# Performance work log

Measured on AMD Instinct MI355X. Metric: run time of the kernel, lower is better.

Reference implementation:

```python
import jax, jax.numpy as jnp
import numpy as np

B, S, D, H = 4, 1024, 1024, 16
HS = D // H  # head_size = 64


def setup_inputs() -> dict:
    key = jax.random.key(0)
    ks = jax.random.split(key, 12)
    sc_d = 1.0 / np.sqrt(D)
    sc_h = 1.0 / np.sqrt(HS)
    inp = {
        "queries": jax.random.normal(ks[0], (B, S, D), jnp.float32),
        "keys": jax.random.normal(ks[1], (B, S, D), jnp.float32),
        "values": jax.random.normal(ks[2], (B, S, D), jnp.float32),
        # causal mask: scores where mask == 0 are filled with -1e9
        "mask": jnp.tril(jnp.ones((S, S), jnp.int32)),
        # per-head query/key projections: [H, D, HS] weights, [H, HS] biases
        "Wq": jax.random.uniform(ks[3], (H, D, HS), jnp.float32, -sc_d, sc_d),
        "bq": jax.random.uniform(ks[4], (H, HS), jnp.float32, -sc_d, sc_d),
        "Wk": jax.random.uniform(ks[5], (H, D, HS), jnp.float32, -sc_d, sc_d),
        "bk": jax.random.uniform(ks[6], (H, HS), jnp.float32, -sc_d, sc_d),
        # shared value projection: [D, HS]
        "Wv": jax.random.uniform(ks[7], (D, HS), jnp.float32, -sc_d, sc_d),
        "bv": jax.random.uniform(ks[8], (HS,), jnp.float32, -sc_d, sc_d),
        # output projection: [HS, D]
        "Wo": jax.random.uniform(ks[9], (HS, D), jnp.float32, -sc_h, sc_h),
        "bo": jax.random.uniform(ks[10], (D,), jnp.float32, -sc_h, sc_h),
    }
    return inp


def reference(queries, keys, values, mask, Wq, bq, Wk, bk, Wv, bv, Wo, bo):
    # shared value projection: [B, S, HS]
    v = jnp.einsum("bsd,de->bse", values, Wv) + bv
    # batched per-head projections (replaces the python loop over heads)
    q = jnp.einsum("bsd,hde->bhse", queries, Wq) + bq[None, :, None, :]
    k = jnp.einsum("btd,hde->bhte", keys, Wk) + bk[None, :, None, :]
    scores = jnp.einsum("bhse,bhte->bhst", q, k) / jnp.sqrt(jnp.float32(HS))
    scores = jnp.where(mask == 0, jnp.float32(-1e9), scores)
    attn = jax.nn.softmax(scores, axis=-1)  # [B, H, S, S]; dropout = eval-mode identity
    head_out = jnp.einsum("bhst,bte->bhse", attn, v)
    out = head_out.mean(axis=1)  # mean over heads -> [B, S, HS]
    out = jnp.einsum("bse,ed->bsd", out, Wo) + bo
    attention_weights = attn.mean(axis=1)  # [B, S, S]
    return out, attention_weights
```

## Files before the change

kernel.cpp:

```cpp
#include <hip/hip_runtime.h>
#include <hip/hip_bf16.h>
#include <stdint.h>

typedef _Float16 half8 __attribute__((ext_vector_type(8)));
typedef _Float16 half4 __attribute__((ext_vector_type(4)));
typedef float    f32x4 __attribute__((ext_vector_type(4)));

#define MFMA16(a, b, c) __builtin_amdgcn_mfma_f32_16x16x32_f16(a, b, c, 0, 0, 0)

__global__ __launch_bounds__(256) void transpose_to_f16(
    const float* __restrict__ X, _Float16* __restrict__ Y,
    int R, int C, long inBS, long outBS)
{
    __shared__ float t[32][33];
    const int bz = blockIdx.z;
    X += (long)bz * inBS;
    Y += (long)bz * outBS;
    const int c0 = blockIdx.x * 32, r0 = blockIdx.y * 32;
    const int tx = threadIdx.x & 31, ty = threadIdx.x >> 5;
#pragma unroll
    for (int i = 0; i < 4; ++i)
        t[ty + i * 8][tx] = X[(long)(r0 + ty + i * 8) * C + c0 + tx];
    __syncthreads();
#pragma unroll
    for (int i = 0; i < 4; ++i)
        Y[(long)(c0 + ty + i * 8) * R + r0 + tx] = (_Float16)t[tx][ty + i * 8];
}

__global__ __launch_bounds__(256, 2) void gemm_f16_v2(
    const float* __restrict__ A0, const float* __restrict__ A1,
    const _Float16* __restrict__ BT,
    const float* __restrict__ bias0, const float* __restrict__ bias1,
    void* __restrict__ Cout,
    int N, int lda, int ldbt, int ldc,
    long aBS, long bBS, long cBS,
    int c_half, int atomic, int nks, int kchunk)
{
    __shared__ __align__(16) _Float16 As[128][72];
    __shared__ __align__(16) _Float16 Bs[128][72];

    const int gx  = gridDim.x, gy = gridDim.y;
    const int nwg = gx * gy * (int)gridDim.z;
    const int lid = (int)blockIdx.x + gx * ((int)blockIdx.y + gy * (int)blockIdx.z);
    const int q8  = nwg >> 3, r8 = nwg & 7;
    const int xcd = lid & 7, loc = lid >> 3;
    const int sw  = (xcd < r8 ? xcd * (q8 + 1) : r8 * (q8 + 1) + (xcd - r8) * q8) + loc;
    const int nt  = sw % gx;
    const int tm2 = sw / gx;
    const int mt  = tm2 % gy;
    const int bz  = tm2 / gy;

    const int b = bz / nks, ks = bz % nks;
    const int kbeg = ks * kchunk;
    const int kend = kbeg + kchunk;

    const float* A = A1 ? (b ? A1 : A0) : (A0 + (long)b * aBS);
    const _Float16* Bb = BT + (long)b * bBS;

    const int n0 = nt * 128;
    const int m0 = mt * 128;
    const int tid  = threadIdx.x;
    const int wave = tid >> 6, lane = tid & 63;
    const int m16  = lane & 15, quad = lane >> 4;

    const int acol = (tid & 15) * 4;
    const int arb  = tid >> 4;
    const int bj   = tid >> 1;
    const int bcc  = (tid & 1) * 32;
    int jn = n0 + bj; if (jn > N - 1) jn = N - 1;
    const _Float16* bpB = Bb + (long)jn * ldbt;

    f32x4 acc[2][8];
    {
        f32x4 z = {0.f, 0.f, 0.f, 0.f};
#pragma unroll
        for (int i = 0; i < 2; ++i)
#pragma unroll
            for (int j = 0; j < 8; ++j) acc[i][j] = z;
    }

    float4 av[8];
    half8  bv0, bv1, bv2, bv3;

    auto LOADT = [&](int k0) {
#pragma unroll
        for (int p = 0; p < 8; ++p)
            av[p] = *(const float4*)(A + (long)(m0 + arb + p * 16) * lda + k0 + acol);
        const _Float16* bp = bpB + k0 + bcc;
        bv0 = *(const half8*)(bp);
        bv1 = *(const half8*)(bp + 8);
        bv2 = *(const half8*)(bp + 16);
        bv3 = *(const half8*)(bp + 24);
    };
    auto STORE_LDS = [&]() {
#pragma unroll
        for (int p = 0; p < 8; ++p) {
            half4 hv;
            hv[0] = (_Float16)av[p].x; hv[1] = (_Float16)av[p].y;
            hv[2] = (_Float16)av[p].z; hv[3] = (_Float16)av[p].w;
            *(half4*)&As[arb + p * 16][acol] = hv;
        }
        *(half8*)&Bs[bj][bcc]      = bv0;
        *(half8*)&Bs[bj][bcc + 8]  = bv1;
        *(half8*)&Bs[bj][bcc + 16] = bv2;
        *(half8*)&Bs[bj][bcc + 24] = bv3;
    };

    LOADT(kbeg);
    for (int k0 = kbeg; k0 < kend; k0 += 64) {
        STORE_LDS();
        __syncthreads();
        if (k0 + 64 < kend) LOADT(k0 + 64);
#pragma unroll
        for (int kss = 0; kss < 2; ++kss) {
            const int ko = kss * 32 + quad * 8;
            const half8 a0 = *(const half8*)&As[wave * 32 + m16][ko];
            const half8 a1 = *(const half8*)&As[wave * 32 + 16 + m16][ko];
#pragma unroll
            for (int c = 0; c < 8; ++c) {
                const half8 bf = *(const half8*)&Bs[c * 16 + m16][ko];
                acc[0][c] = MFMA16(a0, bf, acc[0][c]);
                acc[1][c] = MFMA16(a1, bf, acc[1][c]);
            }
        }
        __syncthreads();
    }

    const float* bias = b ? bias1 : bias0;
    const int addb = (bias != nullptr) && (kbeg == 0);
#pragma unroll
    for (int hh = 0; hh < 2; ++hh) {
#pragma unroll
        for (int c = 0; c < 8; ++c) {
            const int col = n0 + c * 16 + m16;
            if (col >= N) continue;
            const float bb = addb ? bias[col] : 0.f;
#pragma unroll
            for (int r = 0; r < 4; ++r) {
                const int row = m0 + wave * 32 + hh * 16 + quad * 4 + r;
                const float v = acc[hh][c][r] + bb;
                const long idx = (long)b * cBS + (long)row * ldc + col;
                if (atomic)      atomicAdd(&((float*)Cout)[idx], v);
                else if (c_half) ((_Float16*)Cout)[idx] = (_Float16)v;
                else             ((float*)Cout)[idx] = v;
            }
        }
    }
}

__global__ __launch_bounds__(256, 2) void attn_stats(
    const _Float16* __restrict__ q_all, const _Float16* __restrict__ k_all,
    float* __restrict__ m_out, float* __restrict__ il_out)
{
    const int st = blockIdx.x, h = blockIdx.y, b = blockIdx.z;
    const int tid = threadIdx.x, wave = tid >> 6, lane = tid & 63;
    const int m16 = lane & 15, quad = lane >> 4;
    const int s0 = st * 64;
    const int sw = s0 + wave * 16;

    __shared__ __align__(16) _Float16 qs[64][72];
    __shared__ __align__(16) _Float16 ks[64][72];

    const int srow = tid >> 2;
    const int scol = (tid & 3) * 16;

    {
        const _Float16* qsrc = q_all + ((long)(b * 1024 + s0 + srow)) * 1024 + h * 64 + scol;
        *(half8*)&qs[srow][scol]     = *(const half8*)(qsrc);
        *(half8*)&qs[srow][scol + 8] = *(const half8*)(qsrc + 8);
    }

    const _Float16* ksrcb = k_all + ((long)(b * 1024 + srow)) * 1024 + h * 64 + scol;

    float mr[4], lr[4];
#pragma unroll
    for (int r = 0; r < 4; ++r) { mr[r] = -3.0e38f; lr[r] = 0.f; }

    half8 a0, a1;
    for (int tt = 0; tt <= st; ++tt) {
        const _Float16* ksrc = ksrcb + (long)(tt * 64) * 1024;
        const half8 k0 = *(const half8*)(ksrc);
        const half8 k1 = *(const half8*)(ksrc + 8);

        __syncthreads();
        *(half8*)&ks[srow][scol]     = k0;
        *(half8*)&ks[srow][scol + 8] = k1;
        __syncthreads();

        if (tt == 0) {
            a0 = *(const half8*)&qs[wave * 16 + m16][quad * 8];
            a1 = *(const half8*)&qs[wave * 16 + m16][quad * 8 + 32];
        }

        if (tt < st) {
#pragma unroll
            for (int c = 0; c < 4; ++c) {
                const half8 b0 = *(const half8*)&ks[c * 16 + m16][quad * 8];
                const half8 b1 = *(const half8*)&ks[c * 16 + m16][quad * 8 + 32];
                f32x4 cc = {0.f, 0.f, 0.f, 0.f};
                cc = MFMA16(a0, b0, cc);
                cc = MFMA16(a1, b1, cc);
#pragma unroll
                for (int r = 0; r < 4; ++r) {
                    const float z  = cc[r] * 0.125f;
                    const float nm = fmaxf(mr[r], z);
                    lr[r] = lr[r] * __expf(mr[r] - nm) + __expf(z - nm);
                    mr[r] = nm;
                }
            }
        } else {
#pragma unroll
            for (int c = 0; c < 4; ++c) {
                const half8 b0 = *(const half8*)&ks[c * 16 + m16][quad * 8];
                const half8 b1 = *(const half8*)&ks[c * 16 + m16][quad * 8 + 32];
                f32x4 cc = {0.f, 0.f, 0.f, 0.f};
                cc = MFMA16(a0, b0, cc);
                cc = MFMA16(a1, b1, cc);
                const int col = tt * 64 + c * 16 + m16;
#pragma unroll
                for (int r = 0; r < 4; ++r) {
                    const int row = sw + quad * 4 + r;
                    if (col <= row) {
                        const float z  = cc[r] * 0.125f;
                        const float nm = fmaxf(mr[r], z);
                        lr[r] = lr[r] * __expf(mr[r] - nm) + __expf(z - nm);
                        mr[r] = nm;
                    }
                }
            }
        }
    }

#pragma unroll
    for (int mk = 1; mk < 16; mk <<= 1) {
#pragma unroll
        for (int r = 0; r < 4; ++r) {
            const float om = __shfl_xor(mr[r], mk);
            const float ol = __shfl_xor(lr[r], mk);
            const float nm = fmaxf(mr[r], om);
            lr[r] = lr[r] * __expf(mr[r] - nm) + ol * __expf(om - nm);
            mr[r] = nm;
        }
    }
    if (m16 == 0) {
#pragma unroll
        for (int r = 0; r < 4; ++r) {
            const long idx = ((long)(b * 16 + h)) * 1024 + sw + quad * 4 + r;
            m_out[idx]  = mr[r];
            il_out[idx] = 1.f / lr[r];
        }
    }
}

__global__ __launch_bounds__(256, 2) void attn_pmean(
    const _Float16* __restrict__ q_all, const _Float16* __restrict__ k_all,
    const float* __restrict__ m_in, const float* __restrict__ il_in,
    float* __restrict__ attn)
{
    const int ttile = blockIdx.x, stile = blockIdx.y, b = blockIdx.z;
    const int tid = threadIdx.x;
    if (ttile > stile) {
        const int c4 = (tid & 15) * 4;
        float4 z = {0.f, 0.f, 0.f, 0.f};
#pragma unroll
        for (int i = 0; i < 4; ++i) {
            const int r = stile * 64 + (tid >> 4) + i * 16;
            *(float4*)&attn[((long)(b * 1024 + r)) * 1024 + ttile * 64 + c4] = z;
        }
        return;
    }

    __shared__ __align__(16) _Float16 qs[64][72];
    __shared__ __align__(16) _Float16 ks[64][72];

    const int wave = tid >> 6, lane = tid & 63;
    const int m16 = lane & 15, quad = lane >> 4;
    const int s0 = stile * 64;
    const int t0 = ttile * 64;
    const int sw = s0 + wave * 16;
    const int diag = (ttile == stile);

    const int srow = tid >> 2;
    const int scol = (tid & 3) * 16;

    const _Float16* qsrc = q_all + ((long)(b * 1024 + s0 + srow)) * 1024 + scol;
    const _Float16* ksrc = k_all + ((long)(b * 1024 + t0 + srow)) * 1024 + scol;
    const long sbase = ((long)(b * 16)) * 1024 + sw + quad * 4;

    float pm[4][4];
#pragma unroll
    for (int c = 0; c < 4; ++c)
#pragma unroll
        for (int r = 0; r < 4; ++r) pm[c][r] = 0.f;

    for (int h = 0; h < 16; ++h) {
        const int ho = h * 64;
        const half8 q0 = *(const half8*)(qsrc + ho);
        const half8 q1 = *(const half8*)(qsrc + ho + 8);
        const half8 k0 = *(const half8*)(ksrc + ho);
        const half8 k1 = *(const half8*)(ksrc + ho + 8);
        const long idx = sbase + (long)h * 1024;
        const float4 mv = *(const float4*)&m_in[idx];
        const float4 iv = *(const float4*)&il_in[idx];

        __syncthreads();
        *(half8*)&qs[srow][scol]     = q0;
        *(half8*)&qs[srow][scol + 8] = q1;
        *(half8*)&ks[srow][scol]     = k0;
        *(half8*)&ks[srow][scol + 8] = k1;
        __syncthreads();

        const half8 a0 = *(const half8*)&qs[wave * 16 + m16][quad * 8];
        const half8 a1 = *(const half8*)&qs[wave * 16 + m16][quad * 8 + 32];
        const float mrow[4] = {mv.x, mv.y, mv.z, mv.w};
        const float irow[4] = {iv.x, iv.y, iv.z, iv.w};

        if (!diag) {
#pragma unroll
            for (int c = 0; c < 4; ++c) {
                const half8 b0 = *(const half8*)&ks[c * 16 + m16][quad * 8];
                const half8 b1 = *(const half8*)&ks[c * 16 + m16][quad * 8 + 32];
                f32x4 cc = {0.f, 0.f, 0.f, 0.f};
                cc = MFMA16(a0, b0, cc);
                cc = MFMA16(a1, b1, cc);
#pragma unroll
                for (int r = 0; r < 4; ++r)
                    pm[c][r] += __expf(cc[r] * 0.125f - mrow[r]) * irow[r];
            }
        } else {
#pragma unroll
            for (int c = 0; c < 4; ++c) {
                const half8 b0 = *(const half8*)&ks[c * 16 + m16][quad * 8];
                const half8 b1 = *(const half8*)&ks[c * 16 + m16][quad * 8 + 32];
                f32x4 cc = {0.f, 0.f, 0.f, 0.f};
                cc = MFMA16(a0, b0, cc);
                cc = MFMA16(a1, b1, cc);
                const int col = t0 + c * 16 + m16;
#pragma unroll
                for (int r = 0; r < 4; ++r) {
                    const int row = sw + quad * 4 + r;
                    if (col <= row)
                        pm[c][r] += __expf(cc[r] * 0.125f - mrow[r]) * irow[r];
                }
            }
        }
    }

#pragma unroll
    for (int c = 0; c < 4; ++c) {
#pragma unroll
        for (int r = 0; r < 4; ++r) {
            const int row = sw + quad * 4 + r;
            const int col = t0 + c * 16 + m16;
            attn[((long)(b * 1024 + row)) * 1024 + col] = pm[c][r] * 0.0625f;
        }
    }
}

extern "C" void kernel_launch(void* const* d_in, const int* in_sizes, int n_in,
                              void* d_out, int out_size, void* d_ws, size_t ws_size,
                              hipStream_t stream)
{
    const float* queries = (const float*)d_in[0];
    const float* keys    = (const float*)d_in[1];
    const float* values  = (const float*)d_in[2];
    const float* Wq = (const float*)d_in[4];
    const float* bq = (const float*)d_in[5];
    const float* Wk = (const float*)d_in[6];
    const float* bk = (const float*)d_in[7];
    const float* Wv = (const float*)d_in[8];
    const float* bv = (const float*)d_in[9];
    const float* Wo = (const float*)d_in[10];
    const float* bo = (const float*)d_in[11];

    float* out_ptr  = (float*)d_out;
    float* attn_ptr = out_ptr + (long)4096 * 1024;

    uint8_t* w = (uint8_t*)d_ws;
    size_t off = 0;
    auto alloc = [&](size_t bytes) {
        void* p = w + off;
        off = (off + bytes + 255) & ~(size_t)255;
        return p;
    };
    _Float16* WqkT  = (_Float16*)alloc((size_t)2 * 1024 * 1024 * 2);
    _Float16* WvT   = (_Float16*)alloc((size_t)64 * 1024 * 2);
    _Float16* WoT   = (_Float16*)alloc((size_t)1024 * 64 * 2);
    _Float16* qkall = (_Float16*)alloc((size_t)2 * 4194304 * 2);
    float*    vbuf  = (float*)alloc((size_t)4096 * 64 * 4);
    _Float16* vT    = (_Float16*)alloc((size_t)4 * 64 * 1024 * 2);
    float*    ctx   = (float*)alloc((size_t)4096 * 64 * 4);
    float*    mbuf  = (float*)alloc((size_t)65536 * 4);
    float*    ilbuf = (float*)alloc((size_t)65536 * 4);
    (void)ws_size; (void)in_sizes; (void)n_in; (void)out_size;

    _Float16* qall = qkall;
    _Float16* kall = qkall + (long)4194304;

    transpose_to_f16<<<dim3(2, 32, 16), 256, 0, stream>>>(Wq, WqkT, 1024, 64, 65536, 65536);
    transpose_to_f16<<<dim3(2, 32, 16), 256, 0, stream>>>(Wk, WqkT + (long)1024 * 1024, 1024, 64, 65536, 65536);
    transpose_to_f16<<<dim3(2, 32, 1),  256, 0, stream>>>(Wv, WvT, 1024, 64, 0, 0);
    transpose_to_f16<<<dim3(32, 2, 1),  256, 0, stream>>>(Wo, WoT, 64, 1024, 0, 0);

    gemm_f16_v2<<<dim3(8, 32, 2), 256, 0, stream>>>(
        queries, keys, WqkT, bq, bk, qkall,
        1024, 1024, 1024, 1024,
        0, (long)1048576, (long)4194304,
        1, 0, 1, 1024);

    hipMemsetAsync(vbuf, 0, (size_t)4096 * 64 * 4, stream);
    gemm_f16_v2<<<dim3(1, 32, 8), 256, 0, stream>>>(
        values, nullptr, WvT, bv, nullptr, vbuf,
        64, 1024, 1024, 64,
        0, 0, 0,
        0, 1, 8, 128);

    transpose_to_f16<<<dim3(2, 32, 4), 256, 0, stream>>>(vbuf, vT, 1024, 64, 65536, 65536);

    attn_stats<<<dim3(16, 16, 4), 256, 0, stream>>>(qall, kall, mbuf, ilbuf);
    attn_pmean<<<dim3(16, 16, 4), 256, 0, stream>>>(qall, kall, mbuf, ilbuf, attn_ptr);

    hipMemsetAsync(ctx, 0, (size_t)4096 * 64 * 4, stream);
    gemm_f16_v2<<<dim3(1, 8, 32), 256, 0, stream>>>(
        attn_ptr, nullptr, vT, nullptr, nullptr, ctx,
        64, 1024, 1024, 64,
        (long)1048576, (long)65536, (long)65536,
        0, 1, 8, 128);

    gemm_f16_v2<<<dim3(8, 32, 1), 256, 0, stream>>>(
        ctx, nullptr, WoT, bo, nullptr, out_ptr,
        1024, 64, 64, 1024,
        0, 0, 0,
        0, 0, 1, 64);
}
```

Before: 251.7 us.

## Pre-convert Q/K inputs to fp16 and use direct global-to-LDS double-buffered GEMM

Adds a conversion kernel that casts the fp32 query and key activations to fp16 up front. A new QK projection GEMM then streams tiles straight into a swizzled, double-buffered LDS layout via global_load_lds, overlapping the next tile's load with MFMA compute. The generic GEMM also loses its register prefetch and now loads and stores each tile synchronously, which may slow the V and context GEMMs that still use it. The trade-off is an extra read and write of 32MB of fp32 activations plus a new workspace buffer, in exchange for a faster main projection GEMM.

```diff
diff --git a/kernel.cpp b/kernel.cpp
--- a/kernel.cpp
+++ b/kernel.cpp
@@ -7,6 +7,13 @@
 typedef float    f32x4 __attribute__((ext_vector_type(4)));
 
 #define MFMA16(a, b, c) __builtin_amdgcn_mfma_f32_16x16x32_f16(a, b, c, 0, 0, 0)
+
+typedef __attribute__((address_space(1))) const void GVOID;
+typedef __attribute__((address_space(3))) void LVOID;
+__device__ __forceinline__ void glds16(const void* g, void* l)
+{
+    __builtin_amdgcn_global_load_lds((GVOID*)g, (LVOID*)l, 16, 0, 0);
+}
 
 __global__ __launch_bounds__(256) void transpose_to_f16(
     const float* __restrict__ X, _Float16* __restrict__ Y,
@@ -25,6 +32,122 @@
 #pragma unroll
     for (int i = 0; i < 4; ++i)
         Y[(long)(c0 + ty + i * 8) * R + r0 + tx] = (_Float16)t[tx][ty + i * 8];
+}
+
+__global__ __launch_bounds__(256) void cvt_qk_f16(
+    const float* __restrict__ S0, const float* __restrict__ S1,
+    _Float16* __restrict__ D)
+{
+    const float* S = blockIdx.y ? S1 : S0;
+    _Float16* Dz = D + (long)blockIdx.y * 4194304;
+    const long i = ((long)blockIdx.x * 256 + threadIdx.x) * 8;
+    const float4 v0 = *(const float4*)(S + i);
+    const float4 v1 = *(const float4*)(S + i + 4);
+    half8 h;
+    h[0] = (_Float16)v0.x; h[1] = (_Float16)v0.y;
+    h[2] = (_Float16)v0.z; h[3] = (_Float16)v0.w;
+    h[4] = (_Float16)v1.x; h[5] = (_Float16)v1.y;
+    h[6] = (_Float16)v1.z; h[7] = (_Float16)v1.w;
+    *(half8*)(Dz + i) = h;
+}
+
+__global__ __launch_bounds__(256, 2) void gemm_qk_glds(
+    const _Float16* __restrict__ A16,
+    const _Float16* __restrict__ BT,
+    const float* __restrict__ bias0, const float* __restrict__ bias1,
+    _Float16* __restrict__ Cout)
+{
+    __shared__ __align__(16) _Float16 As[2][128 * 64];
+    __shared__ __align__(16) _Float16 Bs[2][128 * 64];
+
+    const int gx  = gridDim.x, gy = gridDim.y;
+    const int nwg = gx * gy * (int)gridDim.z;
+    const int lid = (int)blockIdx.x + gx * ((int)blockIdx.y + gy * (int)blockIdx.z);
+    const int q8  = nwg >> 3;
+    const int xcd = lid & 7, loc = lid >> 3;
+    const int sw  = xcd * q8 + loc;
+    const int nt  = sw % gx;
+    const int tm2 = sw / gx;
+    const int mt  = tm2 % gy;
+    const int z   = tm2 / gy;
+
+    const int n0 = nt * 128;
+    const int m0 = mt * 128;
+    const int tid  = threadIdx.x;
+    const int wave = tid >> 6, lane = tid & 63;
+    const int m16  = lane & 15, quad = lane >> 4;
+
+    const char* Az = (const char*)(A16 + (long)z * 4194304);
+    const char* Bz = (const char*)(BT  + (long)z * 1048576);
+
+    const int colbyte = (((lane & 7) ^ (lane >> 3)) << 4);
+    const char* gaBase = Az + ((long)(m0 + wave * 32 + (lane >> 3)) << 11) + colbyte;
+    const char* gbBase = Bz + ((long)(n0 + wave * 32 + (lane >> 3)) << 11) + colbyte;
+
+    f32x4 acc[2][8];
+    {
+        f32x4 zz = {0.f, 0.f, 0.f, 0.f};
+#pragma unroll
+        for (int i = 0; i < 2; ++i)
+#pragma unroll
+            for (int j = 0; j < 8; ++j) acc[i][j] = zz;
+    }
+
+    auto STAGE = [&](int bf, int k0) {
+        const char* ga = gaBase + (k0 << 1);
+        const char* gb = gbBase + (k0 << 1);
+        _Float16* la = &As[bf][wave * 32 * 64];
+        _Float16* lb = &Bs[bf][wave * 32 * 64];
+#pragma unroll
+        for (int i = 0; i < 4; ++i) {
+            glds16(ga + (long)i * 8 * 2048, la + i * 8 * 64);
+            glds16(gb + (long)i * 8 * 2048, lb + i * 8 * 64);
+        }
+    };
+
+    auto COMPUTE = [&](int bf) {
+        const char* Ab = (const char*)&As[bf][0];
+        const char* Bp = (const char*)&Bs[bf][0];
+        const int sw4 = (m16 & 7) << 4;
+#pragma unroll
+        for (int kss = 0; kss < 2; ++kss) {
+            const int kbs = (kss * 64 + quad * 16) ^ sw4;
+            const half8 a0 = *(const half8*)(Ab + (wave * 32 + m16) * 128 + kbs);
+            const half8 a1 = *(const half8*)(Ab + (wave * 32 + 16 + m16) * 128 + kbs);
+#pragma unroll
+            for (int c = 0; c < 8; ++c) {
+                const half8 bfr = *(const half8*)(Bp + (c * 16 + m16) * 128 + kbs);
+                acc[0][c] = MFMA16(a0, bfr, acc[0][c]);
+                acc[1][c] = MFMA16(a1, bfr, acc[1][c]);
+            }
+        }
+    };
+
+    STAGE(0, 0);
+    __syncthreads();
+    int cur = 0;
+    for (int k0 = 0; k0 < 1024; k0 += 64) {
+        if (k0 + 64 < 1024) STAGE(cur ^ 1, k0 + 64);
+        COMPUTE(cur);
+        __syncthreads();
+        cur ^= 1;
+    }
+
+    const float* bias = z ? bias1 : bias0;
+    _Float16* Cz = Cout + (long)z * 4194304;
+#pragma unroll
+    for (int hh = 0; hh < 2; ++hh) {
+#pragma unroll
+        for (int c = 0; c < 8; ++c) {
+            const int col = n0 + c * 16 + m16;
+            const float bb = bias[col];
+#pragma unroll
+            for (int r = 0; r < 4; ++r) {
+                const int row = m0 + wave * 32 + hh * 16 + quad * 4 + r;
+                Cz[(long)row * 1024 + col] = (_Float16)(acc[hh][c][r] + bb);
+            }
+        }
+    }
 }
 
 __global__ __launch_bounds__(256, 2) void gemm_f16_v2(
@@ -72,45 +195,40 @@
 
     f32x4 acc[2][8];
     {
-        f32x4 z = {0.f, 0.f, 0.f, 0.f};
+        f32x4 zz = {0.f, 0.f, 0.f, 0.f};
 #pragma unroll
         for (int i = 0; i < 2; ++i)
 #pragma unroll
-            for (int j = 0; j < 8; ++j) acc[i][j] = z;
-    }
-
-    float4 av[8];
-    half8  bv0, bv1, bv2, bv3;
-
-    auto LOADT = [&](int k0) {
-#pragma unroll
-        for (int p = 0; p < 8; ++p)
-            av[p] = *(const float4*)(A + (long)(m0 + arb + p * 16) * lda + k0 + acol);
-        const _Float16* bp = bpB + k0 + bcc;
-        bv0 = *(const half8*)(bp);
-        bv1 = *(const half8*)(bp + 8);
-        bv2 = *(const half8*)(bp + 16);
-        bv3 = *(const half8*)(bp + 24);
-    };
-    auto STORE_LDS = [&]() {
-#pragma unroll
-        for (int p = 0; p < 8; ++p) {
-            half4 hv;
-            hv[0] = (_Float16)av[p].x; hv[1] = (_Float16)av[p].y;
-            hv[2] = (_Float16)av[p].z; hv[3] = (_Float16)av[p].w;
-            *(half4*)&As[arb + p * 16][acol] = hv;
-        }
-        *(half8*)&Bs[bj][bcc]      = bv0;
-        *(half8*)&Bs[bj][bcc + 8]  = bv1;
-        *(half8*)&Bs[bj][bcc + 16] = bv2;
-        *(half8*)&Bs[bj][bcc + 24] = bv3;
-    };
-
-    LOADT(kbeg);
+            for (int j = 0; j < 8; ++j) acc[i][j] = zz;
+    }
+
     for (int k0 = kbeg; k0 < kend; k0 += 64) {
-        STORE_LDS();
-        __syncthreads();
-        if (k0 + 64 < kend) LOADT(k0 + 64);
+        {
+            const int cc = acol;
+            float4 av[8];
+#pragma unroll
+            for (int p = 0; p < 8; ++p)
+                av[p] = *(const float4*)(A + (long)(m0 + arb + p * 16) * lda + k0 + cc);
+#pragma unroll
+            for (int p = 0; p < 8; ++p) {
+                half4 hv;
+                hv[0] = (_Float16)av[p].x; hv[1] = (_Float16)av[p].y;
+                hv[2] = (_Float16)av[p].z; hv[3] = (_Float16)av[p].w;
+                *(half4*)&As[arb + p * 16][cc] = hv;
+            }
+        }
+        {
+            const _Float16* bp = bpB + k0 + bcc;
+            half8 b0 = *(const half8*)(bp);
+            half8 b1 = *(const half8*)(bp + 8);
+            half8 b2 = *(const half8*)(bp + 16);
+            half8 b3 = *(const half8*)(bp + 24);
+            *(half8*)&Bs[bj][bcc]      = b0;
+            *(half8*)&Bs[bj][bcc + 8]  = b1;
+            *(half8*)&Bs[bj][bcc + 16] = b2;
+            *(half8*)&Bs[bj][bcc + 24] = b3;
+        }
+        __syncthreads();
 #pragma unroll
         for (int kss = 0; kss < 2; ++kss) {
             const int ko = kss * 32 + quad * 8;
@@ -202,9 +320,9 @@
                 cc = MFMA16(a1, b1, cc);
 #pragma unroll
                 for (int r = 0; r < 4; ++r) {
-                    const float z  = cc[r] * 0.125f;
-                    const float nm = fmaxf(mr[r], z);
-                    lr[r] = lr[r] * __expf(mr[r] - nm) + __expf(z - nm);
+                    const float zz = cc[r] * 0.125f;
+                    const float nm = fmaxf(mr[r], zz);
+                    lr[r] = lr[r] * __expf(mr[r] - nm) + __expf(zz - nm);
                     mr[r] = nm;
                 }
             }
@@ -221,9 +339,9 @@
                 for (int r = 0; r < 4; ++r) {
                     const int row = sw + quad * 4 + r;
                     if (col <= row) {
-                        const float z  = cc[r] * 0.125f;
-                        const float nm = fmaxf(mr[r], z);
-                        lr[r] = lr[r] * __expf(mr[r] - nm) + __expf(z - nm);
+                        const float zz = cc[r] * 0.125f;
+                        const float nm = fmaxf(mr[r], zz);
+                        lr[r] = lr[r] * __expf(mr[r] - nm) + __expf(zz - nm);
                         mr[r] = nm;
                     }
                 }
@@ -261,11 +379,11 @@
     const int tid = threadIdx.x;
     if (ttile > stile) {
         const int c4 = (tid & 15) * 4;
-        float4 z = {0.f, 0.f, 0.f, 0.f};
+        float4 zz = {0.f, 0.f, 0.f, 0.f};
 #pragma unroll
         for (int i = 0; i < 4; ++i) {
             const int r = stile * 64 + (tid >> 4) + i * 16;
-            *(float4*)&attn[((long)(b * 1024 + r)) * 1024 + ttile * 64 + c4] = z;
+            *(float4*)&attn[((long)(b * 1024 + r)) * 1024 + ttile * 64 + c4] = zz;
         }
         return;
     }
@@ -387,6 +505,7 @@
     _Float16* WvT   = (_Float16*)alloc((size_t)64 * 1024 * 2);
     _Float16* WoT   = (_Float16*)alloc((size_t)1024 * 64 * 2);
     _Float16* qkall = (_Float16*)alloc((size_t)2 * 4194304 * 2);
+    _Float16* a16   = (_Float16*)alloc((size_t)2 * 4194304 * 2);
     float*    vbuf  = (float*)alloc((size_t)4096 * 64 * 4);
     _Float16* vT    = (_Float16*)alloc((size_t)4 * 64 * 1024 * 2);
     float*    ctx   = (float*)alloc((size_t)4096 * 64 * 4);
@@ -401,12 +520,10 @@
     transpose_to_f16<<<dim3(2, 32, 16), 256, 0, stream>>>(Wk, WqkT + (long)1024 * 1024, 1024, 64, 65536, 65536);
     transpose_to_f16<<<dim3(2, 32, 1),  256, 0, stream>>>(Wv, WvT, 1024, 64, 0, 0);
     transpose_to_f16<<<dim3(32, 2, 1),  256, 0, stream>>>(Wo, WoT, 64, 1024, 0, 0);
-
-    gemm_f16_v2<<<dim3(8, 32, 2), 256, 0, stream>>>(
-        queries, keys, WqkT, bq, bk, qkall,
-        1024, 1024, 1024, 1024,
-        0, (long)1048576, (long)4194304,
-        1, 0, 1, 1024);
+    cvt_qk_f16<<<dim3(2048, 2, 1), 256, 0, stream>>>(queries, keys, a16);
+
+    gemm_qk_glds<<<dim3(8, 32, 2), 256, 0, stream>>>(
+        a16, WqkT, bq, bk, qkall);
 
     hipMemsetAsync(vbuf, 0, (size_t)4096 * 64 * 4, stream);
     gemm_f16_v2<<<dim3(1, 32, 8), 256, 0, stream>>>(
```

Measured after the change: 252.9 us. Within noise of the previous version (+0.5%).
